# Kernel optimization log

Measured on AMD Instinct MI355X. Metric: run time of the kernel, lower is better.

The kernel has to match this reference:

```python
import jax, jax.numpy as jnp
import numpy as np

KERNELS = (4, 8, 16, 32, 64, 128)  # 2**k for k in (2,3,4,5,6,7)


def _windowed_neg_entropy(x, k):
    # x: [B, C, L] -> windows [B, C, L-k+1, k] via gather (vectorized unfold)
    L = x.shape[-1]
    idx = jnp.arange(L - k + 1)[:, None] + jnp.arange(k)[None, :]  # [W, k]
    t = x[:, :, idx]  # [B, C, W, k]
    # sum(softmax * log_softmax) over window dim (negative entropy), as in torch code
    return jnp.sum(jax.nn.softmax(t, axis=-1) * jax.nn.log_softmax(t, axis=-1), axis=-1)


def setup_inputs() -> dict:
    key = jax.random.key(0)
    k1, k2 = jax.random.split(key)
    input = jax.random.normal(k1, (64, 2, 2048), dtype=jnp.float32)
    target = jax.random.normal(k2, (64, 2, 2048), dtype=jnp.float32)
    return {"input": input, "target": target}


def reference(input, target):
    # L1Loss default reduction is 'mean'; sum losses over all kernel scales
    losses = [jnp.mean(jnp.abs(_windowed_neg_entropy(input, k) - _windowed_neg_entropy(target, k)))
              for k in KERNELS]
    return jnp.sum(jnp.stack(losses))
```

## Files before the change

kernel.cpp:

```cpp
#include <hip/hip_runtime.h>
#include <math.h>

#define LEN 2048
#define NROWS 128
#define NCH 6
#define STRIDE 384
#define LN2 0.69314718055994531f

#define W4   (1.0f / (NROWS * 2045.0f))
#define W8   (1.0f / (NROWS * 2041.0f))
#define W16  (1.0f / (NROWS * 2033.0f))
#define W32  (1.0f / (NROWS * 2017.0f))
#define W64  (1.0f / (NROWS * 1985.0f))
#define W128 (1.0f / (NROWS * 1921.0f))

__global__ __launch_bounds__(512) void entropy_loss_kernel(
    const float* __restrict__ input, const float* __restrict__ target,
    float* __restrict__ out)
{
    const int tid  = threadIdx.x;
    const int lane = tid & 63;
    const int wid  = tid >> 6;
    const int gw   = blockIdx.x * 8 + wid;
    const int row  = gw / NCH;
    const int c    = gw - row * NCH;
    const int base = c * STRIDE;
    const int g0   = base + lane * 8;

    const float* xrow = input  + row * LEN;
    const float* yrow = target + row * LEN;

    const int gb = (g0 <= LEN - 8) ? g0 : (LEN - 8);
    float4 xa = *(const float4*)(xrow + gb);
    float4 xb = *(const float4*)(xrow + gb + 4);
    float4 ya = *(const float4*)(yrow + gb);
    float4 yb = *(const float4*)(yrow + gb + 4);
    float x[8] = {xa.x, xa.y, xa.z, xa.w, xb.x, xb.y, xb.z, xb.w};
    float y[8] = {ya.x, ya.y, ya.z, ya.w, yb.x, yb.y, yb.z, yb.w};
    if (g0 >= LEN) {
        #pragma unroll
        for (int i = 0; i < 8; ++i) { x[i] = -1000.0f; y[i] = -1000.0f; }
    }

    float Ex[11], Sx[11], Ey[11], Sy[11];
    #pragma unroll
    for (int i = 0; i < 8; ++i) {
        Ex[i] = __expf(x[i]); Sx[i] = x[i] * Ex[i];
        Ey[i] = __expf(y[i]); Sy[i] = y[i] * Ey[i];
    }
    #pragma unroll
    for (int i = 0; i < 3; ++i) {
        Ex[8 + i] = __shfl_down(Ex[i], 1);
        Sx[8 + i] = __shfl_down(Sx[i], 1);
        Ey[8 + i] = __shfl_down(Ey[i], 1);
        Sy[8 + i] = __shfl_down(Sy[i], 1);
    }

    float Zx[8], Tx[8], Zy[8], Ty[8];
    #pragma unroll
    for (int s = 0; s < 8; ++s) {
        Zx[s] = (Ex[s] + Ex[s+1]) + (Ex[s+2] + Ex[s+3]);
        Tx[s] = (Sx[s] + Sx[s+1]) + (Sx[s+2] + Sx[s+3]);
        Zy[s] = (Ey[s] + Ey[s+1]) + (Ey[s+2] + Ey[s+3]);
        Ty[s] = (Sy[s] + Sy[s+1]) + (Sy[s+2] + Sy[s+3]);
    }

    float acc = 0.0f;
    const bool owner = (lane < 48);

    auto ne_acc = [&](int k, float w) {
        #pragma unroll
        for (int s = 0; s < 8; ++s) {
            float rx = __builtin_amdgcn_rcpf(Zx[s]);
            float ry = __builtin_amdgcn_rcpf(Zy[s]);
            float d  = fmaf(Tx[s], rx, -Ty[s] * ry) - LN2 * __log2f(Zx[s] * ry);
            if (owner && (g0 + s) <= LEN - k)
                acc = fmaf(w, fabsf(d), acc);
        }
    };

    ne_acc(4, W4);

    {
        float pZx[4], pTx[4], pZy[4], pTy[4];
        #pragma unroll
        for (int s = 0; s < 4; ++s) {
            pZx[s] = __shfl_down(Zx[s], 1);
            pTx[s] = __shfl_down(Tx[s], 1);
            pZy[s] = __shfl_down(Zy[s], 1);
            pTy[s] = __shfl_down(Ty[s], 1);
        }
        #pragma unroll
        for (int s = 0; s < 4; ++s) {
            Zx[s] += Zx[s+4]; Tx[s] += Tx[s+4];
            Zy[s] += Zy[s+4]; Ty[s] += Ty[s+4];
        }
        #pragma unroll
        for (int s = 4; s < 8; ++s) {
            Zx[s] += pZx[s-4]; Tx[s] += pTx[s-4];
            Zy[s] += pZy[s-4]; Ty[s] += pTy[s-4];
        }
        ne_acc(8, W8);
    }

    #pragma unroll
    for (int lev = 0; lev < 4; ++lev) {
        const int d = 1 << lev;
        #pragma unroll
        for (int s = 0; s < 8; ++s) {
            Zx[s] += __shfl_down(Zx[s], d);
            Tx[s] += __shfl_down(Tx[s], d);
            Zy[s] += __shfl_down(Zy[s], d);
            Ty[s] += __shfl_down(Ty[s], d);
        }
        if (d == 1) ne_acc(16, W16);
        if (d == 2) ne_acc(32, W32);
        if (d == 4) ne_acc(64, W64);
        if (d == 8) ne_acc(128, W128);
    }

    #pragma unroll
    for (int off = 32; off > 0; off >>= 1)
        acc += __shfl_down(acc, off);
    __shared__ float red[8];
    if (lane == 0) red[wid] = acc;
    __syncthreads();
    if (tid == 0) {
        float t = ((red[0] + red[1]) + (red[2] + red[3]))
                + ((red[4] + red[5]) + (red[6] + red[7]));
        atomicAdd(out, t);
    }
}

extern "C" void kernel_launch(void* const* d_in, const int* in_sizes, int n_in,
                              void* d_out, int out_size, void* d_ws, size_t ws_size,
                              hipStream_t stream) {
    const float* input  = (const float*)d_in[0];
    const float* target = (const float*)d_in[1];
    float* out = (float*)d_out;

    entropy_loss_kernel<<<dim3(96), dim3(512), 0, stream>>>(input, target, out);
}
```

Baseline: 60.27 us.

## Halve per-lane width to four elements and spread work over more waves

Each lane now handles 4 positions instead of 8, and each row is split into 16 chunks of 128 outputs rather than 6 chunks of 384. The grid grows from 96 to 256 blocks so more CUs and waves are busy and each lane keeps fewer registers. In exchange, the ratio of halo loads to useful work rises (32 of 64 lanes own outputs), and every scale now needs an extra shuffle level.

```diff
diff --git a/kernel.cpp b/kernel.cpp
--- a/kernel.cpp
+++ b/kernel.cpp
@@ -3,8 +3,8 @@
 
 #define LEN 2048
 #define NROWS 128
-#define NCH 6
-#define STRIDE 384
+#define NCH 16
+#define STRIDE 128
 #define LN2 0.69314718055994531f
 
 #define W4   (1.0f / (NROWS * 2045.0f))
@@ -22,43 +22,41 @@
     const int lane = tid & 63;
     const int wid  = tid >> 6;
     const int gw   = blockIdx.x * 8 + wid;
-    const int row  = gw / NCH;
-    const int c    = gw - row * NCH;
+    const int row  = gw >> 4;
+    const int c    = gw & (NCH - 1);
     const int base = c * STRIDE;
-    const int g0   = base + lane * 8;
+    const int g0   = base + lane * 4;
 
     const float* xrow = input  + row * LEN;
     const float* yrow = target + row * LEN;
 
-    const int gb = (g0 <= LEN - 8) ? g0 : (LEN - 8);
+    const int gb = (g0 <= LEN - 4) ? g0 : (LEN - 4);
     float4 xa = *(const float4*)(xrow + gb);
-    float4 xb = *(const float4*)(xrow + gb + 4);
     float4 ya = *(const float4*)(yrow + gb);
-    float4 yb = *(const float4*)(yrow + gb + 4);
-    float x[8] = {xa.x, xa.y, xa.z, xa.w, xb.x, xb.y, xb.z, xb.w};
-    float y[8] = {ya.x, ya.y, ya.z, ya.w, yb.x, yb.y, yb.z, yb.w};
+    float x[4] = {xa.x, xa.y, xa.z, xa.w};
+    float y[4] = {ya.x, ya.y, ya.z, ya.w};
     if (g0 >= LEN) {
         #pragma unroll
-        for (int i = 0; i < 8; ++i) { x[i] = -1000.0f; y[i] = -1000.0f; }
+        for (int i = 0; i < 4; ++i) { x[i] = -1000.0f; y[i] = -1000.0f; }
     }
 
-    float Ex[11], Sx[11], Ey[11], Sy[11];
+    float Ex[7], Sx[7], Ey[7], Sy[7];
     #pragma unroll
-    for (int i = 0; i < 8; ++i) {
+    for (int i = 0; i < 4; ++i) {
         Ex[i] = __expf(x[i]); Sx[i] = x[i] * Ex[i];
         Ey[i] = __expf(y[i]); Sy[i] = y[i] * Ey[i];
     }
     #pragma unroll
     for (int i = 0; i < 3; ++i) {
-        Ex[8 + i] = __shfl_down(Ex[i], 1);
-        Sx[8 + i] = __shfl_down(Sx[i], 1);
-        Ey[8 + i] = __shfl_down(Ey[i], 1);
-        Sy[8 + i] = __shfl_down(Sy[i], 1);
+        Ex[4 + i] = __shfl_down(Ex[i], 1);
+        Sx[4 + i] = __shfl_down(Sx[i], 1);
+        Ey[4 + i] = __shfl_down(Ey[i], 1);
+        Sy[4 + i] = __shfl_down(Sy[i], 1);
     }
 
-    float Zx[8], Tx[8], Zy[8], Ty[8];
+    float Zx[4], Tx[4], Zy[4], Ty[4];
     #pragma unroll
-    for (int s = 0; s < 8; ++s) {
+    for (int s = 0; s < 4; ++s) {
         Zx[s] = (Ex[s] + Ex[s+1]) + (Ex[s+2] + Ex[s+3]);
         Tx[s] = (Sx[s] + Sx[s+1]) + (Sx[s+2] + Sx[s+3]);
         Zy[s] = (Ey[s] + Ey[s+1]) + (Ey[s+2] + Ey[s+3]);
@@ -66,11 +64,11 @@
     }
 
     float acc = 0.0f;
-    const bool owner = (lane < 48);
+    const bool owner = (lane < 32);
 
     auto ne_acc = [&](int k, float w) {
         #pragma unroll
-        for (int s = 0; s < 8; ++s) {
+        for (int s = 0; s < 4; ++s) {
             float rx = __builtin_amdgcn_rcpf(Zx[s]);
             float ry = __builtin_amdgcn_rcpf(Zy[s]);
             float d  = fmaf(Tx[s], rx, -Ty[s] * ry) - LN2 * __log2f(Zx[s] * ry);
@@ -81,42 +79,21 @@
 
     ne_acc(4, W4);
 
-    {
-        float pZx[4], pTx[4], pZy[4], pTy[4];
+    #pragma unroll
+    for (int lev = 0; lev < 5; ++lev) {
+        const int d = 1 << lev;
         #pragma unroll
         for (int s = 0; s < 4; ++s) {
-            pZx[s] = __shfl_down(Zx[s], 1);
-            pTx[s] = __shfl_down(Tx[s], 1);
-            pZy[s] = __shfl_down(Zy[s], 1);
-            pTy[s] = __shfl_down(Ty[s], 1);
-        }
-        #pragma unroll
-        for (int s = 0; s < 4; ++s) {
-            Zx[s] += Zx[s+4]; Tx[s] += Tx[s+4];
-            Zy[s] += Zy[s+4]; Ty[s] += Ty[s+4];
-        }
-        #pragma unroll
-        for (int s = 4; s < 8; ++s) {
-            Zx[s] += pZx[s-4]; Tx[s] += pTx[s-4];
-            Zy[s] += pZy[s-4]; Ty[s] += pTy[s-4];
-        }
-        ne_acc(8, W8);
-    }
-
-    #pragma unroll
-    for (int lev = 0; lev < 4; ++lev) {
-        const int d = 1 << lev;
-        #pragma unroll
-        for (int s = 0; s < 8; ++s) {
             Zx[s] += __shfl_down(Zx[s], d);
             Tx[s] += __shfl_down(Tx[s], d);
             Zy[s] += __shfl_down(Zy[s], d);
             Ty[s] += __shfl_down(Ty[s], d);
         }
-        if (d == 1) ne_acc(16, W16);
-        if (d == 2) ne_acc(32, W32);
-        if (d == 4) ne_acc(64, W64);
-        if (d == 8) ne_acc(128, W128);
+        if (d == 1)  ne_acc(8,   W8);
+        if (d == 2)  ne_acc(16,  W16);
+        if (d == 4)  ne_acc(32,  W32);
+        if (d == 8)  ne_acc(64,  W64);
+        if (d == 16) ne_acc(128, W128);
     }
 
     #pragma unroll
@@ -139,5 +116,5 @@
     const float* target = (const float*)d_in[1];
     float* out = (float*)d_out;
 
-    entropy_loss_kernel<<<dim3(96), dim3(512), 0, stream>>>(input, target, out);
+    entropy_loss_kernel<<<dim3(256), dim3(512), 0, stream>>>(input, target, out);
 }
```

After: 61.39 us. About the same (+1.9%).
